# Optimization experiments

Hardware: AMD Instinct MI355X
Metric: run time of the kernel (lower is better)

## Reference

```python
import jax, jax.numpy as jnp
import numpy as np
from jax import lax

C_IN, C_OUT, K = 32, 32, 3
DIV = float(np.sqrt(C_IN * K * K))  # sqrt(channels_in * filter_size^2)


def setup_inputs() -> dict:
    key = jax.random.key(0)
    kx, kw = jax.random.split(key)
    x = jax.random.normal(kx, (32, C_IN, 256, 256), dtype=jnp.float32)  # NCHW
    # torch.normal(0.0, 0.01, (Cout, Cin, k, k))
    weight = 0.01 * jax.random.normal(kw, (C_OUT, C_IN, K, K), dtype=jnp.float32)
    return {"x": x, "weight": weight}


def reference(x, weight):
    # binarize weights: sign with 0 -> -1 (torch.where(x > 0, 1.0, -1.0))
    weight_bin = jnp.where(weight > 0, 1.0, -1.0).astype(weight.dtype)
    # conv2d with 'same' padding (padding = k // 2, stride 1)
    out = lax.conv_general_dilated(
        x, weight_bin,
        window_strides=(1, 1),
        padding=((K // 2, K // 2), (K // 2, K // 2)),
        dimension_numbers=("NCHW", "OIHW", "NCHW"),
    )
    return out / DIV
```

## Files before the change

kernel.cpp:

```cpp
#include <hip/hip_runtime.h>


typedef __attribute__((ext_vector_type(8))) short short8;
typedef __attribute__((ext_vector_type(4))) float f32x4;

__device__ __forceinline__ short bf16s(float f) {
    unsigned int u = __builtin_bit_cast(unsigned int, f);
    u += 0x7FFFu + ((u >> 16) & 1u);
    return (short)(u >> 16);
}

__global__ __launch_bounds__(512, 4)
void bconv2d_kernel(const float* __restrict__ x, const float* __restrict__ wgt,
                    float* __restrict__ out) {
    __shared__ short8 lds[12 * 264];

    const int tid = threadIdx.x;
    const int gx0 = blockIdx.x * 64;
    const int Y0  = blockIdx.y * 64;
    const int n   = blockIdx.z;

    const int l      = tid & 63;
    const int wv     = tid >> 6;
    const int r      = wv & 3;
    const int ch     = wv >> 2;
    const int lane15 = l & 15;
    const int lhi    = l >> 4;

    short8 afrag[3][3];
    {
        const int co  = ch * 16 + lane15;
        const int ci0 = lhi * 8;
        #pragma unroll
        for (int dy = 0; dy < 3; ++dy)
            #pragma unroll
            for (int dx = 0; dx < 3; ++dx) {
                short8 a;
                #pragma unroll
                for (int j = 0; j < 8; ++j) {
                    float wval = wgt[((co * 32 + ci0 + j) * 3 + dy) * 3 + dx];
                    a[j] = (short)((wval > 0.0f) ? 0x3F80 : 0xBF80);
                }
                afrag[dy][dx] = a;
            }
    }

    const float* xn = x + (size_t)n * 32 * 65536;

    float rg[2][8];
    float re[8];

    auto stage_load = [&](int s) {
        const int bg = Y0 + 4 * s - 1;
        #pragma unroll
        for (int k = 0; k < 2; ++k) {
            const int t  = tid + k * 512;
            const int rr = t >> 8;
            const int u  = (t >> 6) & 3;
            const int pl = 1 + (t & 63);
            const int gy = bg + rr;
            if ((unsigned)gy < 256u) {
                const float* src = xn + ((size_t)(u * 8) * 256 + gy) * 256 + gx0 + (pl - 1);
                #pragma unroll
                for (int j = 0; j < 8; ++j) rg[k][j] = src[(size_t)j * 65536];
            } else {
                #pragma unroll
                for (int j = 0; j < 8; ++j) rg[k][j] = 0.0f;
            }
        }
        if (tid >= 480) {
            const int e    = tid - 480;
            const int rr   = e >> 3;
            const int u    = (e >> 1) & 3;
            const int side = e & 1;
            const int gy   = bg + rr;
            const int gx   = side ? gx0 + 64 : gx0 - 1;
            if ((unsigned)gy < 256u && (unsigned)gx < 256u) {
                const float* src = xn + ((size_t)(u * 8) * 256 + gy) * 256 + gx;
                #pragma unroll
                for (int j = 0; j < 8; ++j) re[j] = src[(size_t)j * 65536];
            } else {
                #pragma unroll
                for (int j = 0; j < 8; ++j) re[j] = 0.0f;
            }
        }
    };

    auto stage_write = [&](int s) {
        const int slot0 = 4 * (s % 3);
        #pragma unroll
        for (int k = 0; k < 2; ++k) {
            const int t  = tid + k * 512;
            const int rr = t >> 8;
            const int u  = (t >> 6) & 3;
            const int pl = 1 + (t & 63);
            short8 v;
            #pragma unroll
            for (int j = 0; j < 8; ++j) v[j] = bf16s(rg[k][j]);
            lds[(slot0 + rr) * 264 + pl * 4 + (u ^ ((pl >> 1) & 3))] = v;
        }
        if (tid >= 480) {
            const int e    = tid - 480;
            const int rr   = e >> 3;
            const int u    = (e >> 1) & 3;
            const int side = e & 1;
            const int pl   = side ? 65 : 0;
            short8 v;
            #pragma unroll
            for (int j = 0; j < 8; ++j) v[j] = bf16s(re[j]);
            lds[(slot0 + rr) * 264 + pl * 4 + (u ^ ((pl >> 1) & 3))] = v;
        }
    };

    stage_load(0);
    stage_write(0);
    stage_load(1);

    const float invdiv = 0.05892556509887896f;
    int i3 = 0;

    for (int i = 0; i < 16; ++i) {
        stage_write(i + 1);
        __syncthreads();
        if (i < 15) stage_load(i + 2);

        f32x4 acc[4];
        #pragma unroll
        for (int tp = 0; tp < 4; ++tp) acc[tp] = (f32x4)0.0f;

        #pragma unroll
        for (int ss = 0; ss < 3; ++ss) {
            int m = 4 * i3 + r + ss;
            if (m >= 12) m -= 12;
            const int sbase = m * 264;
            #pragma unroll
            for (int dx = 0; dx < 3; ++dx)
                #pragma unroll
                for (int tp = 0; tp < 4; ++tp) {
                    const int pl = tp * 16 + lane15 + dx;
                    short8 b = lds[sbase + pl * 4 + (lhi ^ ((pl >> 1) & 3))];
                    acc[tp] = __builtin_amdgcn_mfma_f32_16x16x32_bf16(
                        afrag[ss][dx], b, acc[tp], 0, 0, 0);
                }
        }

        const int y = Y0 + 4 * i + r;
        #pragma unroll
        for (int tp = 0; tp < 4; ++tp)
            #pragma unroll
            for (int q = 0; q < 4; ++q) {
                const int co = ch * 16 + lhi * 4 + q;
                out[(((size_t)n * 32 + co) * 256 + y) * 256 + gx0 + tp * 16 + lane15]
                    = acc[tp][q] * invdiv;
            }

        i3 = (i3 == 2) ? 0 : i3 + 1;
    }
}

extern "C" void kernel_launch(void* const* d_in, const int* in_sizes, int n_in,
                              void* d_out, int out_size, void* d_ws, size_t ws_size,
                              hipStream_t stream) {
    const float* x   = (const float*)d_in[0];
    const float* wgt = (const float*)d_in[1];
    float* out = (float*)d_out;
    (void)d_ws; (void)ws_size;
    dim3 grid(4, 4, 32);
    dim3 block(512);
    bconv2d_kernel<<<grid, block, 0, stream>>>(x, wgt, out);
}
```

Baseline: 150.3 us.

## Switch to full-width row tiles with a four-slot LDS row ring buffer

Each block now owns 16 full 256-pixel-wide rows of one image instead of a 64x64 tile. Input rows are streamed one at a time through a four-slot ring in LDS, and waves are split across column segments and channel halves. This removes the separate column-halo loads and their thread-divergent path, and makes global loads fully contiguous along the row. In exchange, the vertical halo overhead rises (18 rows loaded per 16 computed) and each iteration prefetches only one row ahead.

```diff
diff --git a/kernel.cpp b/kernel.cpp
--- a/kernel.cpp
+++ b/kernel.cpp
@@ -13,17 +13,17 @@
 __global__ __launch_bounds__(512, 4)
 void bconv2d_kernel(const float* __restrict__ x, const float* __restrict__ wgt,
                     float* __restrict__ out) {
-    __shared__ short8 lds[12 * 264];
+    __shared__ short8 lds[4 * 1032];
 
     const int tid = threadIdx.x;
-    const int gx0 = blockIdx.x * 64;
-    const int Y0  = blockIdx.y * 64;
-    const int n   = blockIdx.z;
+    const int y0  = blockIdx.x * 16;
+    const int n   = blockIdx.y;
 
     const int l      = tid & 63;
     const int wv     = tid >> 6;
-    const int r      = wv & 3;
-    const int ch     = wv >> 2;
+    const int seg    = wv >> 1;
+    const int ch     = wv & 1;
+    const int px0    = seg * 64;
     const int lane15 = l & 15;
     const int lhi    = l >> 4;
 
@@ -48,81 +48,57 @@
     const float* xn = x + (size_t)n * 32 * 65536;
 
     float rg[2][8];
-    float re[8];
 
-    auto stage_load = [&](int s) {
-        const int bg = Y0 + 4 * s - 1;
+    auto load_row = [&](int gy) {
+        if ((unsigned)gy < 256u) {
+            #pragma unroll
+            for (int k = 0; k < 2; ++k) {
+                const int t  = tid + k * 512;
+                const int u  = t >> 8;
+                const int gx = t & 255;
+                const float* src = xn + ((size_t)(u * 8) * 256 + gy) * 256 + gx;
+                #pragma unroll
+                for (int j = 0; j < 8; ++j) rg[k][j] = src[(size_t)j * 65536];
+            }
+        } else {
+            #pragma unroll
+            for (int k = 0; k < 2; ++k)
+                #pragma unroll
+                for (int j = 0; j < 8; ++j) rg[k][j] = 0.0f;
+        }
+    };
+
+    auto write_row = [&](int slot) {
         #pragma unroll
         for (int k = 0; k < 2; ++k) {
             const int t  = tid + k * 512;
-            const int rr = t >> 8;
-            const int u  = (t >> 6) & 3;
-            const int pl = 1 + (t & 63);
-            const int gy = bg + rr;
-            if ((unsigned)gy < 256u) {
-                const float* src = xn + ((size_t)(u * 8) * 256 + gy) * 256 + gx0 + (pl - 1);
-                #pragma unroll
-                for (int j = 0; j < 8; ++j) rg[k][j] = src[(size_t)j * 65536];
-            } else {
-                #pragma unroll
-                for (int j = 0; j < 8; ++j) rg[k][j] = 0.0f;
-            }
-        }
-        if (tid >= 480) {
-            const int e    = tid - 480;
-            const int rr   = e >> 3;
-            const int u    = (e >> 1) & 3;
-            const int side = e & 1;
-            const int gy   = bg + rr;
-            const int gx   = side ? gx0 + 64 : gx0 - 1;
-            if ((unsigned)gy < 256u && (unsigned)gx < 256u) {
-                const float* src = xn + ((size_t)(u * 8) * 256 + gy) * 256 + gx;
-                #pragma unroll
-                for (int j = 0; j < 8; ++j) re[j] = src[(size_t)j * 65536];
-            } else {
-                #pragma unroll
-                for (int j = 0; j < 8; ++j) re[j] = 0.0f;
-            }
+            const int u  = t >> 8;
+            const int pl = 1 + (t & 255);
+            short8 v;
+            #pragma unroll
+            for (int j = 0; j < 8; ++j) v[j] = bf16s(rg[k][j]);
+            lds[slot * 1032 + pl * 4 + (u ^ ((pl >> 1) & 3))] = v;
         }
     };
 
-    auto stage_write = [&](int s) {
-        const int slot0 = 4 * (s % 3);
-        #pragma unroll
-        for (int k = 0; k < 2; ++k) {
-            const int t  = tid + k * 512;
-            const int rr = t >> 8;
-            const int u  = (t >> 6) & 3;
-            const int pl = 1 + (t & 63);
-            short8 v;
-            #pragma unroll
-            for (int j = 0; j < 8; ++j) v[j] = bf16s(rg[k][j]);
-            lds[(slot0 + rr) * 264 + pl * 4 + (u ^ ((pl >> 1) & 3))] = v;
-        }
-        if (tid >= 480) {
-            const int e    = tid - 480;
-            const int rr   = e >> 3;
-            const int u    = (e >> 1) & 3;
-            const int side = e & 1;
-            const int pl   = side ? 65 : 0;
-            short8 v;
-            #pragma unroll
-            for (int j = 0; j < 8; ++j) v[j] = bf16s(re[j]);
-            lds[(slot0 + rr) * 264 + pl * 4 + (u ^ ((pl >> 1) & 3))] = v;
-        }
-    };
-
-    stage_load(0);
-    stage_write(0);
-    stage_load(1);
+    load_row(y0 - 1); write_row((y0 - 1) & 3);
+    load_row(y0);     write_row(y0 & 3);
+    load_row(y0 + 1); write_row((y0 + 1) & 3);
+    if (tid < 32) {
+        const int slot = tid & 3;
+        const int u    = (tid >> 2) & 3;
+        const int pl   = (tid >> 4) ? 257 : 0;
+        lds[slot * 1032 + pl * 4 + u] = (short8)0;
+    }
+    __syncthreads();
 
     const float invdiv = 0.05892556509887896f;
-    int i3 = 0;
 
-    for (int i = 0; i < 16; ++i) {
-        stage_write(i + 1);
-        __syncthreads();
-        if (i < 15) stage_load(i + 2);
+    #pragma unroll 4
+    for (int yy = 0; yy < 16; ++yy) {
+        const int y = y0 + yy;
+
+        load_row(y + 2);
 
         f32x4 acc[4];
         #pragma unroll
@@ -130,31 +106,31 @@
 
         #pragma unroll
         for (int ss = 0; ss < 3; ++ss) {
-            int m = 4 * i3 + r + ss;
-            if (m >= 12) m -= 12;
-            const int sbase = m * 264;
+            const int m     = (yy + ss + 3) & 3;
+            const int sbase = m * 1032;
             #pragma unroll
             for (int dx = 0; dx < 3; ++dx)
                 #pragma unroll
                 for (int tp = 0; tp < 4; ++tp) {
-                    const int pl = tp * 16 + lane15 + dx;
+                    const int pl = px0 + tp * 16 + lane15 + dx;
                     short8 b = lds[sbase + pl * 4 + (lhi ^ ((pl >> 1) & 3))];
                     acc[tp] = __builtin_amdgcn_mfma_f32_16x16x32_bf16(
                         afrag[ss][dx], b, acc[tp], 0, 0, 0);
                 }
         }
 
-        const int y = Y0 + 4 * i + r;
+        write_row((yy + 2) & 3);
+
         #pragma unroll
         for (int tp = 0; tp < 4; ++tp)
             #pragma unroll
             for (int q = 0; q < 4; ++q) {
                 const int co = ch * 16 + lhi * 4 + q;
-                out[(((size_t)n * 32 + co) * 256 + y) * 256 + gx0 + tp * 16 + lane15]
+                out[(((size_t)n * 32 + co) * 256 + y) * 256 + px0 + tp * 16 + lane15]
                     = acc[tp][q] * invdiv;
             }
 
-        i3 = (i3 == 2) ? 0 : i3 + 1;
+        __syncthreads();
     }
 }
 
@@ -165,7 +141,7 @@
     const float* wgt = (const float*)d_in[1];
     float* out = (float*)d_out;
     (void)d_ws; (void)ws_size;
-    dim3 grid(4, 4, 32);
+    dim3 grid(16, 32);
     dim3 block(512);
     bconv2d_kernel<<<grid, block, 0, stream>>>(x, wgt, out);
 }
```

Measured after the change: 140.0 us. 1.07x faster.
